# Kernel tuning notes

Hardware: AMD Instinct MI355X
Metric: run time of the kernel (lower is better)

The kernel has to match this reference:

```python
import jax, jax.numpy as jnp
import numpy as np

FILTER_LEN = 1024
HOP_LEN = 256


def _forward_basis(filter_len):
    half = filter_len // 2 + 1
    basis = np.fft.fft(np.eye(filter_len))
    basis = np.vstack([np.real(basis[:half, :]), np.imag(basis[:half, :])])
    # hann window, fftbins=True (periodic)
    n = np.arange(filter_len)
    win = 0.5 - 0.5 * np.cos(2.0 * np.pi * n / filter_len)
    return (basis * win).astype(np.float32)  # [2*half, filter_len]


def setup_inputs() -> dict:
    key = jax.random.key(0)
    x = jax.random.normal(key, (8, 1048576), dtype=jnp.float32)
    basis = jnp.asarray(_forward_basis(FILTER_LEN))[:, None, :]  # [O=1026, I=1, K=1024]
    return {"x": x, "basis": basis}


def reference(x, basis):
    pad = FILTER_LEN // 2
    # [B, 1, T + filter_len] with reflect padding on the time axis
    xp = jnp.pad(x[:, None, :], ((0, 0), (0, 0), (pad, pad)), mode="reflect")
    # strided conv1d against the fixed DFT basis -> [B, 1026, n_frames]
    out = jax.lax.conv_general_dilated(
        xp, basis,
        window_strides=(HOP_LEN,),
        padding="VALID",
        dimension_numbers=("NCH", "OIH", "NCH"),
    )
    return out
```

## Files before the change

kernel.cpp:

```cpp
#include <hip/hip_runtime.h>
#include <hip/hip_bf16.h>

#define T_LEN 1048576
#define FL    1024
#define PADL  512
#define HOP   256
#define NFR   4097
#define NB    8
#define XP2   1049600
#define NSEG  4100
#define MROWS 1028
#define MPAD  1152
#define MTL   18
#define FTL   34
#define NTL   272
#define NWG2  4896

typedef __bf16 bf16x8 __attribute__((ext_vector_type(8)));
typedef float  f32x4  __attribute__((ext_vector_type(4)));

__device__ __forceinline__ void gload16(const __hip_bfloat16* g, void* l) {
  __builtin_amdgcn_global_load_lds(
      (const __attribute__((address_space(1))) unsigned int*)g,
      (__attribute__((address_space(3))) unsigned int*)l, 16, 0, 0);
}

__global__ __launch_bounds__(256) void pad_convert_x8(
    const float* __restrict__ x, __hip_bfloat16* __restrict__ xp) {
  const int base = (blockIdx.x * 256 + threadIdx.x) * 8;
  const int b = blockIdx.y;
  if (base >= XP2) return;
  const float* __restrict__ xb = x + (size_t)b * T_LEN;
  union { bf16x8 v; __hip_bfloat16 h[8]; } o;
  if (base >= PADL && base + 8 <= PADL + T_LEN) {
    const float4 v0 = *(const float4*)&xb[base - PADL];
    const float4 v1 = *(const float4*)&xb[base - PADL + 4];
    o.h[0] = __float2bfloat16(v0.x); o.h[1] = __float2bfloat16(v0.y);
    o.h[2] = __float2bfloat16(v0.z); o.h[3] = __float2bfloat16(v0.w);
    o.h[4] = __float2bfloat16(v1.x); o.h[5] = __float2bfloat16(v1.y);
    o.h[6] = __float2bfloat16(v1.z); o.h[7] = __float2bfloat16(v1.w);
    *(bf16x8*)&xp[(size_t)b * XP2 + base] = o.v;
  } else {
    for (int e = 0; e < 8; ++e) {
      const int i = base + e;
      if (i < XP2) {
        const int t = i - PADL;
        const int idx = (t < 0) ? -t : ((t >= T_LEN) ? (2 * T_LEN - 2 - t) : t);
        xp[(size_t)b * XP2 + i] = __float2bfloat16(xb[idx]);
      }
    }
  }
}

__global__ __launch_bounds__(256) void build_cmat(__hip_bfloat16* __restrict__ cm) {
  const int idx = blockIdx.x * 256 + threadIdx.x;
  if (idx >= MPAD * 256) return;
  const int row = idx >> 8, r = idx & 255;
  float v = 0.f;
  if (row < MROWS) {
    const int k = row >> 1;
    const int ph = (k * r) & 1023;
    const float ang = (float)ph * 6.2831853071795864769f / 1024.f;
    v = (row & 1) ? -sinf(ang) : cosf(ang);
  }
  cm[idx] = __float2bfloat16(v);
}

__global__ __launch_bounds__(512, 3) void stft_fgemm(
    const __hip_bfloat16* __restrict__ Cm,
    const __hip_bfloat16* __restrict__ X,
    float* __restrict__ out) {
  __shared__ char ldsraw[49152];
  __hip_bfloat16* stg = (__hip_bfloat16*)ldsraw;
  float* Ub = (float*)ldsraw;

  const int orig = blockIdx.x;
  const int wg = (orig & 7) * (NWG2 / 8) + (orig >> 3);
  const int mt = wg % MTL;
  const int nt = wg / MTL;
  const int b = nt / FTL, ft = nt % FTL;
  const int gb = ft * 124;
  const int RB = mt * 60;
  const int kbase = 30 * mt;

  const int tid = threadIdx.x;
  const int w = tid >> 6, l = tid & 63;
  const bool isProd = w >= 4;
  const int cw = w & 3;
  const int wm = cw >> 1, wn = cw & 1;

  const int g_log = (l & 3) ^ ((l >> 3) & 3);
  const int srow = l >> 2;
  const __hip_bfloat16* aB0 = Cm + (size_t)(RB + cw * 16 + srow) * 256 + g_log * 8;
  const __hip_bfloat16* bB_[2];
#pragma unroll
  for (int j = 0; j < 2; ++j) {
    int g = gb + (cw * 2 + j) * 16 + srow;
    if (g > NSEG - 1) g = NSEG - 1;
    bB_[j] = X + (size_t)b * XP2 + (size_t)g * 256 + g_log * 8;
  }

  const int swz = ((l >> 4) ^ ((l >> 1) & 3)) * 8;
  const int aIdx = (wm * 32 + (l & 15)) * 32 + swz;
  const int bIdx = 2048 + (wn * 64 + (l & 15)) * 32 + swz;

  f32x4 acc[2][4] = {};

#define STAGE(K0_, S_) do {                                                  \
    gload16(aB0 + (K0_), (void*)(stg + (S_) * 6144 + cw * 512));             \
    _Pragma("unroll") for (int j = 0; j < 2; ++j)                            \
      gload16(bB_[j] + (K0_),                                                \
              (void*)(stg + (S_) * 6144 + 2048 + (cw * 2 + j) * 512));       \
  } while (0)

#define RDMM(S_) do {                                                        \
    bf16x8 af_[2], bf_[4];                                                   \
    _Pragma("unroll") for (int m = 0; m < 2; ++m)                            \
      af_[m] = *(const bf16x8*)(stg + (S_) * 6144 + aIdx + m * 512);         \
    _Pragma("unroll") for (int n = 0; n < 4; ++n)                            \
      bf_[n] = *(const bf16x8*)(stg + (S_) * 6144 + bIdx + n * 512);         \
    __builtin_amdgcn_s_setprio(1);                                           \
    _Pragma("unroll") for (int m = 0; m < 2; ++m)                            \
      _Pragma("unroll") for (int n = 0; n < 4; ++n)                          \
        acc[m][n] = __builtin_amdgcn_mfma_f32_16x16x32_bf16(                 \
            bf_[n], af_[m], acc[m][n], 0, 0, 0);                             \
    __builtin_amdgcn_s_setprio(0);                                           \
  } while (0)

#define BAR __builtin_amdgcn_s_barrier()
#define SB  __builtin_amdgcn_sched_barrier(0)
#define VMC(N_) asm volatile("s_waitcnt vmcnt(" #N_ ")" ::: "memory")

  if (isProd) {
    STAGE(0, 0); STAGE(32, 1); STAGE(64, 2); STAGE(96, 3);
    VMC(6);  BAR;
    VMC(0);  BAR;
    SB; STAGE(128, 0); STAGE(160, 1);
    VMC(0);  BAR;
    SB; STAGE(192, 2); STAGE(224, 3);
    VMC(0);  BAR;
  } else {
    BAR;
    SB; RDMM(0); RDMM(1); BAR;
    SB; RDMM(2); RDMM(3); BAR;
    SB; RDMM(0); RDMM(1); BAR;
    SB; RDMM(2); RDMM(3);
  }
  __syncthreads();

#undef VMC
#undef SB
#undef RDMM
#undef STAGE

  if (!isProd) {
    const int cb = l & 15, fb4 = (l >> 4) * 4;
#pragma unroll
    for (int m = 0; m < 2; ++m)
#pragma unroll
      for (int n = 0; n < 4; ++n) {
        const int row = wm * 32 + m * 16 + cb;
        const int col = wn * 64 + n * 16 + fb4;
        *(f32x4*)(Ub + row * 132 + col) = acc[m][n];
      }
  }
  __syncthreads();

  f32x4 zre[2], zim[2];
#pragma unroll
  for (int it = 0; it < 2; ++it) {
    const int cell = it * 512 + tid;
    const int rp = cell >> 5;
    const int g4 = (cell & 31) * 4;
    const float* rr = Ub + (rp * 2) * 132 + g4;
    const f32x4 r0 = *(const f32x4*)rr;
    const f32x4 r1 = *(const f32x4*)(rr + 4);
    const f32x4 i0 = *(const f32x4*)(rr + 132);
    const f32x4 i1 = *(const f32x4*)(rr + 136);
    const float ur[8] = {r0[0], r0[1], r0[2], r0[3], r1[0], r1[1], r1[2], r1[3]};
    const float ui[8] = {i0[0], i0[1], i0[2], i0[3], i1[0], i1[1], i1[2], i1[3]};
    const int cls = (kbase + rp) & 3;
    const float s = (cls & 2) ? -1.f : 1.f;
    const bool odd = cls & 1;
    f32x4 zr, zi;
#pragma unroll
    for (int j = 0; j < 4; ++j) {
      const float p  = ur[j] - ur[j + 2], q  = ur[j] + ur[j + 2];
      const float pi = ui[j] - ui[j + 2], qi = ui[j] + ui[j + 2];
      const float rm = ur[j + 1] - ur[j + 3], rp_ = ur[j + 1] + ur[j + 3];
      const float sm = ui[j + 1] - ui[j + 3], sp = ui[j + 1] + ui[j + 3];
      zr[j] = odd ? (p + s * sm) : (q + s * rp_);
      zi[j] = odd ? (pi - s * rm) : (qi + s * sp);
    }
    zre[it] = zr; zim[it] = zi;
  }
  __syncthreads();
#pragma unroll
  for (int it = 0; it < 2; ++it) {
    const int cell = it * 512 + tid;
    const int rp = cell >> 5;
    const int g4 = (cell & 31) * 4;
    *(f32x4*)(Ub + (rp * 2) * 132 + g4) = zre[it];
    *(f32x4*)(Ub + (rp * 2 + 1) * 132 + g4) = zim[it];
  }
  __syncthreads();

  const size_t ob = (size_t)b * 1026 * 4097;
#pragma unroll
  for (int it = 0; it < 2; ++it) {
    const int cell = it * 512 + tid;
    const int rp = cell >> 5;
    const int g4 = (cell & 31) * 4;
    const int k = kbase + rp;
    const int f0 = gb + g4;
    if (g4 <= 120) {
      if (rp >= 1 && rp <= 30 && k <= 512) {
        const float* zp = Ub + rp * 264 + g4;
        const f32x4 zmr = *(const f32x4*)(zp - 264);
        const f32x4 zmi = *(const f32x4*)(zp - 132);
        const f32x4 zpr = *(const f32x4*)(zp + 264);
        const f32x4 zpi = *(const f32x4*)(zp + 396);
        const f32x4 Yr = 0.5f * zre[it] - 0.25f * (zmr + zpr);
        const f32x4 Yi = 0.5f * zim[it] - 0.25f * (zmi + zpi);
        float* orow = out + ob + (size_t)k * NFR;
        float* irow = out + ob + (size_t)(513 + k) * NFR;
        if (f0 + 3 <= NFR - 1) {
          *(f32x4*)&orow[f0] = Yr;
          *(f32x4*)&irow[f0] = Yi;
        } else {
#pragma unroll
          for (int j = 0; j < 4; ++j)
            if (f0 + j <= NFR - 1) { orow[f0 + j] = Yr[j]; irow[f0 + j] = Yi[j]; }
        }
      } else if (mt == 0 && rp == 0) {
        const f32x4 z1r = *(const f32x4*)(Ub + 264 + g4);
        const f32x4 Yr = 0.5f * zre[it] - 0.5f * z1r;
        const f32x4 Yi = 0.5f * zim[it];
        if (f0 + 3 <= NFR - 1) {
          *(f32x4*)&out[ob + f0] = Yr;
          *(f32x4*)&out[ob + (size_t)513 * NFR + f0] = Yi;
        } else {
#pragma unroll
          for (int j = 0; j < 4; ++j)
            if (f0 + j <= NFR - 1) {
              out[ob + f0 + j] = Yr[j];
              out[ob + (size_t)513 * NFR + f0 + j] = Yi[j];
            }
        }
      }
    }
  }
#undef BAR
}

extern "C" void kernel_launch(void* const* d_in, const int* in_sizes, int n_in,
                              void* d_out, int out_size, void* d_ws, size_t ws_size,
                              hipStream_t stream) {
  const float* x = (const float*)d_in[0];
  float* out = (float*)d_out;

  __hip_bfloat16* xpBf = (__hip_bfloat16*)d_ws;
  __hip_bfloat16* cmat = xpBf + (size_t)NB * XP2;

  dim3 gPad((XP2 / 8 + 255) / 256, NB);
  pad_convert_x8<<<gPad, 256, 0, stream>>>(x, xpBf);

  build_cmat<<<(MPAD * 256) / 256, 256, 0, stream>>>(cmat);

  stft_fgemm<<<NWG2, 512, 0, stream>>>(cmat, xpBf, out);
}
```

Before: 58.25 us.

## Fuse reflect-pad and bf16 conversion of the signal into the GEMM producer

Removes the separate pad/convert kernel and its padded bf16 workspace. Producer waves now read fp32 samples straight from x, handle reflect-padding at the edges with reversed scalar loads, convert to bf16 and write into the LDS stage with ordinary stores. The aim is to save one kernel launch and a full write-plus-read of the padded signal. In exchange, the producers lose async global-to-LDS loads for B, read twice the bytes per element, and wait on the loads before converting, which shortens the pipeline depth (pairs of stages instead of four in flight).

Result: slower. 161.4 us (+177.1%).

```diff
diff --git a/kernel.cpp b/kernel.cpp
--- a/kernel.cpp
+++ b/kernel.cpp
@@ -7,7 +7,6 @@
 #define HOP   256
 #define NFR   4097
 #define NB    8
-#define XP2   1049600
 #define NSEG  4100
 #define MROWS 1028
 #define MPAD  1152
@@ -25,34 +24,7 @@
       (__attribute__((address_space(3))) unsigned int*)l, 16, 0, 0);
 }
 
-__global__ __launch_bounds__(256) void pad_convert_x8(
-    const float* __restrict__ x, __hip_bfloat16* __restrict__ xp) {
-  const int base = (blockIdx.x * 256 + threadIdx.x) * 8;
-  const int b = blockIdx.y;
-  if (base >= XP2) return;
-  const float* __restrict__ xb = x + (size_t)b * T_LEN;
-  union { bf16x8 v; __hip_bfloat16 h[8]; } o;
-  if (base >= PADL && base + 8 <= PADL + T_LEN) {
-    const float4 v0 = *(const float4*)&xb[base - PADL];
-    const float4 v1 = *(const float4*)&xb[base - PADL + 4];
-    o.h[0] = __float2bfloat16(v0.x); o.h[1] = __float2bfloat16(v0.y);
-    o.h[2] = __float2bfloat16(v0.z); o.h[3] = __float2bfloat16(v0.w);
-    o.h[4] = __float2bfloat16(v1.x); o.h[5] = __float2bfloat16(v1.y);
-    o.h[6] = __float2bfloat16(v1.z); o.h[7] = __float2bfloat16(v1.w);
-    *(bf16x8*)&xp[(size_t)b * XP2 + base] = o.v;
-  } else {
-    for (int e = 0; e < 8; ++e) {
-      const int i = base + e;
-      if (i < XP2) {
-        const int t = i - PADL;
-        const int idx = (t < 0) ? -t : ((t >= T_LEN) ? (2 * T_LEN - 2 - t) : t);
-        xp[(size_t)b * XP2 + i] = __float2bfloat16(xb[idx]);
-      }
-    }
-  }
-}
-
-__global__ __launch_bounds__(256) void build_cmat(__hip_bfloat16* __restrict__ cm) {
+__global__ __launch_bounds__(256) void prep_cmat(__hip_bfloat16* __restrict__ cm) {
   const int idx = blockIdx.x * 256 + threadIdx.x;
   if (idx >= MPAD * 256) return;
   const int row = idx >> 8, r = idx & 255;
@@ -68,7 +40,7 @@
 
 __global__ __launch_bounds__(512, 3) void stft_fgemm(
     const __hip_bfloat16* __restrict__ Cm,
-    const __hip_bfloat16* __restrict__ X,
+    const float* __restrict__ x,
     float* __restrict__ out) {
   __shared__ char ldsraw[49152];
   __hip_bfloat16* stg = (__hip_bfloat16*)ldsraw;
@@ -92,12 +64,17 @@
   const int g_log = (l & 3) ^ ((l >> 3) & 3);
   const int srow = l >> 2;
   const __hip_bfloat16* aB0 = Cm + (size_t)(RB + cw * 16 + srow) * 256 + g_log * 8;
-  const __hip_bfloat16* bB_[2];
+  const float* __restrict__ xb = x + (size_t)b * T_LEN;
+  long boff[2];
+  int edgeC[2];
+  bool intr[2];
 #pragma unroll
   for (int j = 0; j < 2; ++j) {
     int g = gb + (cw * 2 + j) * 16 + srow;
     if (g > NSEG - 1) g = NSEG - 1;
-    bB_[j] = X + (size_t)b * XP2 + (size_t)g * 256 + g_log * 8;
+    intr[j] = (g >= 2 && g <= 4097);
+    boff[j] = (long)g * 256 - 512 + g_log * 8;
+    edgeC[j] = (g <= 1 ? 512 - g * 256 : 2097662 - g * 256) - g_log * 8;
   }
 
   const int swz = ((l >> 4) ^ ((l >> 1) & 3)) * 8;
@@ -105,13 +82,6 @@
   const int bIdx = 2048 + (wn * 64 + (l & 15)) * 32 + swz;
 
   f32x4 acc[2][4] = {};
-
-#define STAGE(K0_, S_) do {                                                  \
-    gload16(aB0 + (K0_), (void*)(stg + (S_) * 6144 + cw * 512));             \
-    _Pragma("unroll") for (int j = 0; j < 2; ++j)                            \
-      gload16(bB_[j] + (K0_),                                                \
-              (void*)(stg + (S_) * 6144 + 2048 + (cw * 2 + j) * 512));       \
-  } while (0)
 
 #define RDMM(S_) do {                                                        \
     bf16x8 af_[2], bf_[4];                                                   \
@@ -129,16 +99,50 @@
 
 #define BAR __builtin_amdgcn_s_barrier()
 #define SB  __builtin_amdgcn_sched_barrier(0)
-#define VMC(N_) asm volatile("s_waitcnt vmcnt(" #N_ ")" ::: "memory")
 
   if (isProd) {
-    STAGE(0, 0); STAGE(32, 1); STAGE(64, 2); STAGE(96, 3);
-    VMC(6);  BAR;
-    VMC(0);  BAR;
-    SB; STAGE(128, 0); STAGE(160, 1);
-    VMC(0);  BAR;
-    SB; STAGE(192, 2); STAGE(224, 3);
-    VMC(0);  BAR;
+#define LDBCH(j_, K0_, F0_, F1_) do {                                        \
+      if (intr[j_]) {                                                        \
+        F0_ = *(const float4*)&xb[boff[j_] + (K0_)];                         \
+        F1_ = *(const float4*)&xb[boff[j_] + (K0_) + 4];                     \
+      } else {                                                               \
+        const int c0_ = edgeC[j_] - (K0_);                                   \
+        F0_.x = xb[c0_];     F0_.y = xb[c0_ - 1];                            \
+        F0_.z = xb[c0_ - 2]; F0_.w = xb[c0_ - 3];                            \
+        F1_.x = xb[c0_ - 4]; F1_.y = xb[c0_ - 5];                            \
+        F1_.z = xb[c0_ - 6]; F1_.w = xb[c0_ - 7];                            \
+      }                                                                      \
+    } while (0)
+
+#define CVTWR(S_, j_, F0_, F1_) do {                                         \
+      union { bf16x8 v; __hip_bfloat16 h[8]; } u_;                           \
+      u_.h[0] = __float2bfloat16(F0_.x); u_.h[1] = __float2bfloat16(F0_.y);  \
+      u_.h[2] = __float2bfloat16(F0_.z); u_.h[3] = __float2bfloat16(F0_.w);  \
+      u_.h[4] = __float2bfloat16(F1_.x); u_.h[5] = __float2bfloat16(F1_.y);  \
+      u_.h[6] = __float2bfloat16(F1_.z); u_.h[7] = __float2bfloat16(F1_.w);  \
+      *(bf16x8*)(stg + (S_) * 6144 + 2048 + (cw * 2 + (j_)) * 512 + l * 8)   \
+          = u_.v;                                                            \
+    } while (0)
+
+#define PAIR(Ka_, Kb_, Sa_, Sb_) do {                                        \
+      float4 f0, f1, f2, f3, h0, h1, h2, h3;                                 \
+      gload16(aB0 + (Ka_), (void*)(stg + (Sa_) * 6144 + cw * 512));          \
+      gload16(aB0 + (Kb_), (void*)(stg + (Sb_) * 6144 + cw * 512));          \
+      LDBCH(0, Ka_, f0, f1); LDBCH(1, Ka_, f2, f3);                          \
+      LDBCH(0, Kb_, h0, h1); LDBCH(1, Kb_, h2, h3);                          \
+      asm volatile("s_waitcnt vmcnt(0)" ::: "memory");                       \
+      CVTWR(Sa_, 0, f0, f1); CVTWR(Sa_, 1, f2, f3);                          \
+      CVTWR(Sb_, 0, h0, h1); CVTWR(Sb_, 1, h2, h3);                          \
+      asm volatile("s_waitcnt lgkmcnt(0)" ::: "memory");                     \
+    } while (0)
+
+    PAIR(0, 32, 0, 1);    BAR;
+    SB; PAIR(64, 96, 2, 3);   BAR;
+    SB; PAIR(128, 160, 0, 1); BAR;
+    SB; PAIR(192, 224, 2, 3); BAR;
+#undef PAIR
+#undef CVTWR
+#undef LDBCH
   } else {
     BAR;
     SB; RDMM(0); RDMM(1); BAR;
@@ -148,10 +152,8 @@
   }
   __syncthreads();
 
-#undef VMC
 #undef SB
 #undef RDMM
-#undef STAGE
 
   if (!isProd) {
     const int cb = l & 15, fb4 = (l >> 4) * 4;
@@ -259,13 +261,8 @@
   const float* x = (const float*)d_in[0];
   float* out = (float*)d_out;
 
-  __hip_bfloat16* xpBf = (__hip_bfloat16*)d_ws;
-  __hip_bfloat16* cmat = xpBf + (size_t)NB * XP2;
-
-  dim3 gPad((XP2 / 8 + 255) / 256, NB);
-  pad_convert_x8<<<gPad, 256, 0, stream>>>(x, xpBf);
-
-  build_cmat<<<(MPAD * 256) / 256, 256, 0, stream>>>(cmat);
-
-  stft_fgemm<<<NWG2, 512, 0, stream>>>(cmat, xpBf, out);
-}
+  __hip_bfloat16* cmat = (__hip_bfloat16*)d_ws;
+
+  prep_cmat<<<MPAD, 256, 0, stream>>>(cmat);
+  stft_fgemm<<<NWG2, 512, 0, stream>>>(cmat, x, out);
+}
```
